# Kernel optimization log

Measured on AMD Instinct MI355X. Metric: run time of the kernel, lower is better.

The kernel has to match this reference:

```python
import jax, jax.numpy as jnp
import numpy as np

NUM_SRC = 200000
NUM_DST = 100000
NUM_EDGES = 1600000
IN_DIM = 128
HID = 256
OUT_DIM = 128


def layer_norm(h, g, b, eps=1e-5):
    mu = jnp.mean(h, axis=-1, keepdims=True)
    var = jnp.mean((h - mu) ** 2, axis=-1, keepdims=True)
    return (h - mu) * jax.lax.rsqrt(var + eps) * g + b


def setup_inputs() -> dict:
    key = jax.random.key(0)
    ks = jax.random.split(key, 8)
    s_in = 1.0 / np.sqrt(IN_DIM)
    s_hid = 1.0 / np.sqrt(HID)
    return {
        "x": jax.random.normal(ks[0], (NUM_SRC, IN_DIM), dtype=jnp.float32),
        "w_l": jax.random.normal(ks[1], (IN_DIM, HID), dtype=jnp.float32) * s_in,
        "b_l": jnp.zeros((HID,), dtype=jnp.float32),
        "w_r": jax.random.normal(ks[2], (IN_DIM, HID), dtype=jnp.float32) * s_in,
        "ln1_g": jnp.ones((HID,), dtype=jnp.float32),
        "ln1_b": jnp.zeros((HID,), dtype=jnp.float32),
        "w_out": jax.random.normal(ks[3], (HID, OUT_DIM), dtype=jnp.float32) * s_hid,
        "b_out": jnp.zeros((OUT_DIM,), dtype=jnp.float32),
        "ln2_g": jnp.ones((OUT_DIM,), dtype=jnp.float32),
        "ln2_b": jnp.zeros((OUT_DIM,), dtype=jnp.float32),
        "edge_src": jax.random.randint(ks[4], (NUM_EDGES,), 0, NUM_SRC, dtype=jnp.int64),
        "edge_dst": jax.random.randint(ks[5], (NUM_EDGES,), 0, NUM_DST, dtype=jnp.int64),
    }


def reference(x, w_l, b_l, w_r, ln1_g, ln1_b, w_out, b_out, ln2_g, ln2_b, edge_src, edge_dst):
    # SAGEConv bipartite: targets are the first NUM_DST rows of x
    x_tgt = x[:NUM_DST]
    # mean aggregation of source-node messages at destination nodes
    msgs = x[edge_src]  # [E, IN_DIM] irregular gather
    summed = jax.ops.segment_sum(msgs, edge_dst, num_segments=NUM_DST)
    cnt = jax.ops.segment_sum(jnp.ones((NUM_EDGES,), dtype=x.dtype), edge_dst, num_segments=NUM_DST)
    mean_nbr = summed / jnp.maximum(cnt, 1.0)[:, None]
    # out = lin_l(aggr) + lin_r(x_target); dropout p=0 is identity
    h = mean_nbr @ w_l + b_l + x_tgt @ w_r
    h = layer_norm(h, ln1_g, ln1_b)
    h = jax.nn.gelu(h, approximate=False)
    out = h @ w_out + b_out
    out = layer_norm(out, ln2_g, ln2_b)
    return out
```

## Files before the change

kernel.cpp:

```cpp
#include <hip/hip_runtime.h>
#include <math.h>

#define NSRC 200000
#define NDST 100000
#define NEDGE 1600000

typedef unsigned int uint32;
typedef unsigned short u16;

typedef short short8 __attribute__((ext_vector_type(8)));
typedef float f32x4 __attribute__((ext_vector_type(4)));

__device__ __forceinline__ u16 f2b(float f) {
  uint32 u = __float_as_uint(f);
  u += 0x7fffu + ((u >> 16) & 1u);
  return (u16)(u >> 16);
}
__device__ __forceinline__ float b2f_lo(uint32 u) { return __uint_as_float(u << 16); }
__device__ __forceinline__ float b2f_hi(uint32 u) { return __uint_as_float(u & 0xffff0000u); }

#define NBKT 1563
#define BKTCAP 1344
#define NB_H 256
#define EPH (NEDGE / NB_H)
#define NB_W 384
#define NB_CVT 25000

__global__ __launch_bounds__(256) void k_prep(const float* __restrict__ x, u16* __restrict__ xb,
                                              const float* __restrict__ wl,
                                              const float* __restrict__ wr,
                                              const float* __restrict__ wo,
                                              u16* __restrict__ wp1f, u16* __restrict__ wp2f,
                                              const int do_cvt, const int* __restrict__ src,
                                              const int* __restrict__ dst,
                                              int* __restrict__ bktcnt,
                                              int* __restrict__ pairs) {
  __shared__ int hist[NBKT];
  __shared__ int loff[NBKT];
  if (blockIdx.x < NB_H) {
    int base = blockIdx.x * EPH;
    for (int i = threadIdx.x; i < NBKT; i += 256) hist[i] = 0;
    __syncthreads();
    for (int i = threadIdx.x; i < EPH; i += 256) atomicAdd(&hist[dst[base + i] >> 6], 1);
    __syncthreads();
    for (int i = threadIdx.x; i < NBKT; i += 256) {
      int h = hist[i];
      loff[i] = h ? atomicAdd(&bktcnt[i * 16], h) : 0;
      hist[i] = 0;
    }
    __syncthreads();
    for (int i = threadIdx.x; i < EPH; i += 256) {
      int d = dst[base + i];
      int s = src[base + i];
      int bin = d >> 6;
      int r = atomicAdd(&hist[bin], 1);
      int pos = loff[bin] + r;
      if (pos < BKTCAP) pairs[(size_t)bin * BKTCAP + pos] = (s << 6) | (d & 63);
    }
    return;
  }
  int bid = blockIdx.x - NB_H;
  if (bid < NB_W) {
    int t = bid * 256 + threadIdx.x;
    if (t < 65536) {
      int j = t & 7, lane = (t >> 3) & 63, nt = (t >> 9) & 3, kc = (t >> 11) & 7, w = t >> 14;
      int k = kc * 32 + (lane >> 4) * 8 + j;
      int n = w * 64 + nt * 16 + (lane & 15);
      float v = (k < 128) ? wl[k * 256 + n] : wr[(k - 128) * 256 + n];
      wp1f[t] = f2b(v);
    } else {
      int t2 = t - 65536;
      int j = t2 & 7, lane = (t2 >> 3) & 63, nt = (t2 >> 9) & 1, kc = (t2 >> 10) & 7, w = t2 >> 13;
      int k = kc * 32 + (lane >> 4) * 8 + j;
      int n = w * 32 + nt * 16 + (lane & 15);
      wp2f[t2] = f2b(wo[k * 128 + n]);
    }
    return;
  }
  if (!do_cvt) return;
  int idx = (bid - NB_W) * 256 + threadIdx.x;
  size_t i = (size_t)idx * 4;
  if (i < (size_t)NSRC * 128) {
    float4 f = *(const float4*)(x + i);
    uint2 o;
    o.x = (uint32)f2b(f.x) | ((uint32)f2b(f.y) << 16);
    o.y = (uint32)f2b(f.z) | ((uint32)f2b(f.w) << 16);
    *(uint2*)(xb + i) = o;
  }
}

#define LDAH 264
#define LCSR_LD 65

__global__ __launch_bounds__(256) void k_fused(
    const u16* __restrict__ xb, const float* __restrict__ xf, const int x_is_bf16,
    const int* __restrict__ pairs, const int* __restrict__ bktcnt,
    const u16* __restrict__ wp1f, const u16* __restrict__ wp2f,
    const float* __restrict__ bl_g, const float* __restrict__ g1_g, const float* __restrict__ b1_g,
    const float* __restrict__ bo_g, const float* __restrict__ g2_g, const float* __restrict__ b2_g,
    float* __restrict__ out) {
  __shared__ __align__(16) u16 AH_lds[64 * LDAH];
  __shared__ float2 stats[4][64];
  __shared__ float2 stats2[64];
  __shared__ int lcnt[64];
  __shared__ int lcsr[64 * LCSR_LD];

  const int tid = threadIdx.x;
  const int wave = tid >> 6;
  const int lane = tid & 63;
  const int l15 = lane & 15;
  const int q = lane >> 4;
  const int row0 = blockIdx.x * 64;

  {
    const int bkt = blockIdx.x;
    int total = bktcnt[(size_t)bkt * 16];
    int mp = total < BKTCAP ? total : BKTCAP;
    if (tid < 64) lcnt[tid] = 0;
    __syncthreads();
    for (int i = tid; i < mp; i += 256) {
      int v = pairs[(size_t)bkt * BKTCAP + i];
      int d6 = v & 63;
      int p = atomicAdd(&lcnt[d6], 1);
      if (p < 64) lcsr[d6 * LCSR_LD + p] = v >> 6;
    }
    __syncthreads();
  }

  {
    const int sub = tid & 15;
    const int dgrp = tid >> 4;
#pragma unroll 1
    for (int pass = 0; pass < 4; pass++) {
      int r = pass * 16 + dgrp;
      int d = row0 + r;
      u16* rowp = AH_lds + r * LDAH;
      if (d < NDST) {
        int n = lcnt[r];
        int m = n < 64 ? n : 64;
        const int* cp = lcsr + r * LCSR_LD;
        float a[8] = {0, 0, 0, 0, 0, 0, 0, 0};
        uint4 xv;
        float4 xf0, xf1;
        if (x_is_bf16) {
          xv = *(const uint4*)(xb + (size_t)d * 128 + sub * 8);
        } else {
          const float* p = xf + (size_t)d * 128 + sub * 8;
          xf0 = *(const float4*)p;
          xf1 = *(const float4*)(p + 4);
        }
        if (x_is_bf16) {
          int i = 0;
          for (; i + 7 < m; i += 8) {
            uint4 p[8];
#pragma unroll
            for (int u = 0; u < 8; u++)
              p[u] = *(const uint4*)(xb + (size_t)cp[i + u] * 128 + sub * 8);
#pragma unroll
            for (int u = 0; u < 8; u++) {
              a[0] += b2f_lo(p[u].x); a[1] += b2f_hi(p[u].x);
              a[2] += b2f_lo(p[u].y); a[3] += b2f_hi(p[u].y);
              a[4] += b2f_lo(p[u].z); a[5] += b2f_hi(p[u].z);
              a[6] += b2f_lo(p[u].w); a[7] += b2f_hi(p[u].w);
            }
          }
          for (; i + 3 < m; i += 4) {
            uint4 p[4];
#pragma unroll
            for (int u = 0; u < 4; u++)
              p[u] = *(const uint4*)(xb + (size_t)cp[i + u] * 128 + sub * 8);
#pragma unroll
            for (int u = 0; u < 4; u++) {
              a[0] += b2f_lo(p[u].x); a[1] += b2f_hi(p[u].x);
              a[2] += b2f_lo(p[u].y); a[3] += b2f_hi(p[u].y);
              a[4] += b2f_lo(p[u].z); a[5] += b2f_hi(p[u].z);
              a[6] += b2f_lo(p[u].w); a[7] += b2f_hi(p[u].w);
            }
          }
          for (; i < m; i++) {
            uint4 p = *(const uint4*)(xb + (size_t)cp[i] * 128 + sub * 8);
            a[0] += b2f_lo(p.x); a[1] += b2f_hi(p.x);
            a[2] += b2f_lo(p.y); a[3] += b2f_hi(p.y);
            a[4] += b2f_lo(p.z); a[5] += b2f_hi(p.z);
            a[6] += b2f_lo(p.w); a[7] += b2f_hi(p.w);
          }
        } else {
          for (int i = 0; i < m; i++) {
            int s = cp[i];
            const float* p = xf + (size_t)s * 128 + sub * 8;
            float4 f0 = *(const float4*)p;
            float4 f1 = *(const float4*)(p + 4);
            a[0] += f0.x; a[1] += f0.y; a[2] += f0.z; a[3] += f0.w;
            a[4] += f1.x; a[5] += f1.y; a[6] += f1.z; a[7] += f1.w;
          }
        }
        float sc = 1.f / (float)(n > 0 ? n : 1);
        uint4 o;
        o.x = (uint32)f2b(a[0] * sc) | ((uint32)f2b(a[1] * sc) << 16);
        o.y = (uint32)f2b(a[2] * sc) | ((uint32)f2b(a[3] * sc) << 16);
        o.z = (uint32)f2b(a[4] * sc) | ((uint32)f2b(a[5] * sc) << 16);
        o.w = (uint32)f2b(a[6] * sc) | ((uint32)f2b(a[7] * sc) << 16);
        *(uint4*)(rowp + sub * 8) = o;
        if (!x_is_bf16) {
          xv.x = (uint32)f2b(xf0.x) | ((uint32)f2b(xf0.y) << 16);
          xv.y = (uint32)f2b(xf0.z) | ((uint32)f2b(xf0.w) << 16);
          xv.z = (uint32)f2b(xf1.x) | ((uint32)f2b(xf1.y) << 16);
          xv.w = (uint32)f2b(xf1.z) | ((uint32)f2b(xf1.w) << 16);
        }
        *(uint4*)(rowp + 128 + sub * 8) = xv;
      } else {
        uint4 z = {0u, 0u, 0u, 0u};
        *(uint4*)(rowp + sub * 8) = z;
        *(uint4*)(rowp + 128 + sub * 8) = z;
      }
    }
  }
  __syncthreads();

  f32x4 acc[4][4];
#pragma unroll
  for (int i = 0; i < 4; i++)
#pragma unroll
    for (int j = 0; j < 4; j++) acc[i][j] = (f32x4){0.f, 0.f, 0.f, 0.f};

#pragma unroll 2
  for (int kc = 0; kc < 8; kc++) {
    short8 bfr[4];
    const uint4* bsrc = (const uint4*)(wp1f + (((size_t)wave * 8 + kc) * 4) * 512);
#pragma unroll
    for (int nt = 0; nt < 4; nt++) bfr[nt] = ((const short8*)(bsrc + nt * 64))[lane];
    short8 af[4];
#pragma unroll
    for (int mt = 0; mt < 4; mt++)
      af[mt] = *(const short8*)(AH_lds + (16 * mt + l15) * LDAH + kc * 32 + q * 8);
#pragma unroll
    for (int mt = 0; mt < 4; mt++)
#pragma unroll
      for (int nt = 0; nt < 4; nt++)
        acc[mt][nt] = __builtin_amdgcn_mfma_f32_16x16x32_bf16(af[mt], bfr[nt], acc[mt][nt], 0, 0, 0);
  }

  float bl[4], g1[4], b1[4];
#pragma unroll
  for (int nt = 0; nt < 4; nt++) {
    int c = 64 * wave + 16 * nt + l15;
    bl[nt] = bl_g[c]; g1[nt] = g1_g[c]; b1[nt] = b1_g[c];
  }
#pragma unroll
  for (int mt = 0; mt < 4; mt++)
#pragma unroll
    for (int nt = 0; nt < 4; nt++)
#pragma unroll
      for (int r = 0; r < 4; r++) acc[mt][nt][r] += bl[nt];

#pragma unroll
  for (int mt = 0; mt < 4; mt++)
#pragma unroll
    for (int r = 0; r < 4; r++) {
      float s = 0.f, s2 = 0.f;
#pragma unroll
      for (int nt = 0; nt < 4; nt++) { float v = acc[mt][nt][r]; s += v; s2 += v * v; }
#pragma unroll
      for (int m = 1; m < 16; m <<= 1) { s += __shfl_xor(s, m, 64); s2 += __shfl_xor(s2, m, 64); }
      if (l15 == 0) stats[wave][16 * mt + 4 * q + r] = make_float2(s, s2);
    }
  __syncthreads();
  if (tid < 64) {
    float S = 0.f, Q = 0.f;
#pragma unroll
    for (int w = 0; w < 4; w++) { float2 t = stats[w][tid]; S += t.x; Q += t.y; }
    float mu = S * (1.f / 256.f);
    float var = Q * (1.f / 256.f) - mu * mu;
    stats2[tid] = make_float2(mu, rsqrtf(var + 1e-5f));
  }
  __syncthreads();
#pragma unroll
  for (int mt = 0; mt < 4; mt++)
#pragma unroll
    for (int r = 0; r < 4; r++) {
      int row = 16 * mt + 4 * q + r;
      float2 st = stats2[row];
#pragma unroll
      for (int nt = 0; nt < 4; nt++) {
        float v = acc[mt][nt][r];
        float hn = (v - st.x) * st.y * g1[nt] + b1[nt];
        float t2 = hn * hn;
        float u = fmaf(0.044715f * t2, hn, hn);
        float ge = hn / (1.f + __expf(-1.5957691216f * u));
        AH_lds[row * LDAH + 64 * wave + 16 * nt + l15] = f2b(ge);
      }
    }
  __syncthreads();

  f32x4 acc2[4][2];
#pragma unroll
  for (int i = 0; i < 4; i++)
#pragma unroll
    for (int j = 0; j < 2; j++) acc2[i][j] = (f32x4){0.f, 0.f, 0.f, 0.f};

#pragma unroll 2
  for (int kc = 0; kc < 8; kc++) {
    short8 bfr[2];
    const uint4* bsrc = (const uint4*)(wp2f + (((size_t)wave * 8 + kc) * 2) * 512);
#pragma unroll
    for (int nt = 0; nt < 2; nt++) bfr[nt] = ((const short8*)(bsrc + nt * 64))[lane];
    short8 af[4];
#pragma unroll
    for (int mt = 0; mt < 4; mt++)
      af[mt] = *(const short8*)(AH_lds + (16 * mt + l15) * LDAH + kc * 32 + q * 8);
#pragma unroll
    for (int mt = 0; mt < 4; mt++)
#pragma unroll
      for (int nt = 0; nt < 2; nt++)
        acc2[mt][nt] = __builtin_amdgcn_mfma_f32_16x16x32_bf16(af[mt], bfr[nt], acc2[mt][nt], 0, 0, 0);
  }

  float bo[2], g2[2], b2c[2];
#pragma unroll
  for (int nt = 0; nt < 2; nt++) {
    int c = 32 * wave + 16 * nt + l15;
    bo[nt] = bo_g[c]; g2[nt] = g2_g[c]; b2c[nt] = b2_g[c];
  }
#pragma unroll
  for (int mt = 0; mt < 4; mt++)
#pragma unroll
    for (int nt = 0; nt < 2; nt++)
#pragma unroll
      for (int r = 0; r < 4; r++) acc2[mt][nt][r] += bo[nt];

#pragma unroll
  for (int mt = 0; mt < 4; mt++)
#pragma unroll
    for (int r = 0; r < 4; r++) {
      float s = 0.f, s2 = 0.f;
#pragma unroll
      for (int nt = 0; nt < 2; nt++) { float v = acc2[mt][nt][r]; s += v; s2 += v * v; }
#pragma unroll
      for (int m = 1; m < 16; m <<= 1) { s += __shfl_xor(s, m, 64); s2 += __shfl_xor(s2, m, 64); }
      if (l15 == 0) stats[wave][16 * mt + 4 * q + r] = make_float2(s, s2);
    }
  __syncthreads();
  if (tid < 64) {
    float S = 0.f, Q = 0.f;
#pragma unroll
    for (int w = 0; w < 4; w++) { float2 t = stats[w][tid]; S += t.x; Q += t.y; }
    float mu = S * (1.f / 128.f);
    float var = Q * (1.f / 128.f) - mu * mu;
    stats2[tid] = make_float2(mu, rsqrtf(var + 1e-5f));
  }
  __syncthreads();
#pragma unroll
  for (int mt = 0; mt < 4; mt++)
#pragma unroll
    for (int r = 0; r < 4; r++) {
      int row = 16 * mt + 4 * q + r;
      int R = row0 + row;
      if (R < NDST) {
        float2 st = stats2[row];
#pragma unroll
        for (int nt = 0; nt < 2; nt++) {
          float v = acc2[mt][nt][r];
          out[(size_t)R * 128 + 32 * wave + 16 * nt + l15] = (v - st.x) * st.y * g2[nt] + b2c[nt];
        }
      }
    }
}

extern "C" void kernel_launch(void* const* d_in, const int* in_sizes, int n_in,
                              void* d_out, int out_size, void* d_ws, size_t ws_size,
                              hipStream_t stream) {
  const float* x   = (const float*)d_in[0];
  const float* w_l = (const float*)d_in[1];
  const float* b_l = (const float*)d_in[2];
  const float* w_r = (const float*)d_in[3];
  const float* g1  = (const float*)d_in[4];
  const float* b1  = (const float*)d_in[5];
  const float* w_o = (const float*)d_in[6];
  const float* b_o = (const float*)d_in[7];
  const float* g2  = (const float*)d_in[8];
  const float* b2  = (const float*)d_in[9];
  const int* esrc  = (const int*)d_in[10];
  const int* edst  = (const int*)d_in[11];
  float* out = (float*)d_out;

  char* ws = (char*)d_ws;
  size_t off = 0;
  auto alloc = [&](size_t bytes) -> void* {
    off = (off + 255) & ~(size_t)255;
    void* p = ws + off;
    off += bytes;
    return p;
  };
  int* bktcnt = (int*)alloc((size_t)NBKT * 16 * 4);
  u16* wp1f   = (u16*)alloc((size_t)65536 * 2);
  u16* wp2f   = (u16*)alloc((size_t)32768 * 2);
  int* pairs  = (int*)alloc((size_t)NBKT * BKTCAP * 4);

  size_t rem = (ws_size > off + 512) ? (ws_size - off - 512) : 0;
  size_t xb_bytes = (size_t)NSRC * 128 * 2;
  int x_is_bf16 = (rem >= xb_bytes) ? 1 : 0;
  u16* xb = x_is_bf16 ? (u16*)alloc(xb_bytes) : nullptr;

  hipMemsetAsync(bktcnt, 0, (size_t)NBKT * 16 * 4, stream);
  k_prep<<<NB_H + NB_W + NB_CVT, 256, 0, stream>>>(x, xb, w_l, w_r, w_o, wp1f, wp2f,
                                                   x_is_bf16, esrc, edst, bktcnt, pairs);
  k_fused<<<NBKT, 256, 0, stream>>>(xb, x, x_is_bf16, pairs, bktcnt, wp1f, wp2f,
                                    b_l, g1, b1, b_o, g2, b2, out);
}
```

Before: 368.5 us.

## Use 512-thread blocks with 2x4 wave grid in fused SAGE kernel

Doubles the fused kernel's block size to 8 waves. The 64-row tile is split into two 32-row halves across wave rows, so each wave holds half the accumulators and the gather loop runs two passes instead of four. Per-row LayerNorm stats are reorganized into an 8x32 layout. The intent is more gather parallelism per bucket and lower register pressure, which should raise occupancy. The cost is that each wave now reloads the same B-fragment weights for only half the M-tiles, and more threads take part in each barrier.

After: 355.6 us. -3.5%, faster.

```diff
diff --git a/kernel.cpp b/kernel.cpp
--- a/kernel.cpp
+++ b/kernel.cpp
@@ -92,7 +92,7 @@
 #define LDAH 264
 #define LCSR_LD 65
 
-__global__ __launch_bounds__(256) void k_fused(
+__global__ __launch_bounds__(512, 6) void k_fused(
     const u16* __restrict__ xb, const float* __restrict__ xf, const int x_is_bf16,
     const int* __restrict__ pairs, const int* __restrict__ bktcnt,
     const u16* __restrict__ wp1f, const u16* __restrict__ wp2f,
@@ -100,7 +100,7 @@
     const float* __restrict__ bo_g, const float* __restrict__ g2_g, const float* __restrict__ b2_g,
     float* __restrict__ out) {
   __shared__ __align__(16) u16 AH_lds[64 * LDAH];
-  __shared__ float2 stats[4][64];
+  __shared__ float2 stats[8][32];
   __shared__ float2 stats2[64];
   __shared__ int lcnt[64];
   __shared__ int lcsr[64 * LCSR_LD];
@@ -110,6 +110,8 @@
   const int lane = tid & 63;
   const int l15 = lane & 15;
   const int q = lane >> 4;
+  const int wr = wave >> 2;
+  const int wc = wave & 3;
   const int row0 = blockIdx.x * 64;
 
   {
@@ -118,7 +120,7 @@
     int mp = total < BKTCAP ? total : BKTCAP;
     if (tid < 64) lcnt[tid] = 0;
     __syncthreads();
-    for (int i = tid; i < mp; i += 256) {
+    for (int i = tid; i < mp; i += 512) {
       int v = pairs[(size_t)bkt * BKTCAP + i];
       int d6 = v & 63;
       int p = atomicAdd(&lcnt[d6], 1);
@@ -131,8 +133,8 @@
     const int sub = tid & 15;
     const int dgrp = tid >> 4;
 #pragma unroll 1
-    for (int pass = 0; pass < 4; pass++) {
-      int r = pass * 16 + dgrp;
+    for (int pass = 0; pass < 2; pass++) {
+      int r = pass * 32 + dgrp;
       int d = row0 + r;
       u16* rowp = AH_lds + r * LDAH;
       if (d < NDST) {
@@ -217,24 +219,24 @@
   }
   __syncthreads();
 
-  f32x4 acc[4][4];
-#pragma unroll
-  for (int i = 0; i < 4; i++)
+  f32x4 acc[2][4];
+#pragma unroll
+  for (int i = 0; i < 2; i++)
 #pragma unroll
     for (int j = 0; j < 4; j++) acc[i][j] = (f32x4){0.f, 0.f, 0.f, 0.f};
 
-#pragma unroll 2
+#pragma unroll 1
   for (int kc = 0; kc < 8; kc++) {
     short8 bfr[4];
-    const uint4* bsrc = (const uint4*)(wp1f + (((size_t)wave * 8 + kc) * 4) * 512);
+    const uint4* bsrc = (const uint4*)(wp1f + (((size_t)wc * 8 + kc) * 4) * 512);
 #pragma unroll
     for (int nt = 0; nt < 4; nt++) bfr[nt] = ((const short8*)(bsrc + nt * 64))[lane];
-    short8 af[4];
-#pragma unroll
-    for (int mt = 0; mt < 4; mt++)
-      af[mt] = *(const short8*)(AH_lds + (16 * mt + l15) * LDAH + kc * 32 + q * 8);
-#pragma unroll
-    for (int mt = 0; mt < 4; mt++)
+    short8 af[2];
+#pragma unroll
+    for (int mt = 0; mt < 2; mt++)
+      af[mt] = *(const short8*)(AH_lds + (32 * wr + 16 * mt + l15) * LDAH + kc * 32 + q * 8);
+#pragma unroll
+    for (int mt = 0; mt < 2; mt++)
 #pragma unroll
       for (int nt = 0; nt < 4; nt++)
         acc[mt][nt] = __builtin_amdgcn_mfma_f32_16x16x32_bf16(af[mt], bfr[nt], acc[mt][nt], 0, 0, 0);
@@ -243,18 +245,18 @@
   float bl[4], g1[4], b1[4];
 #pragma unroll
   for (int nt = 0; nt < 4; nt++) {
-    int c = 64 * wave + 16 * nt + l15;
+    int c = 64 * wc + 16 * nt + l15;
     bl[nt] = bl_g[c]; g1[nt] = g1_g[c]; b1[nt] = b1_g[c];
   }
 #pragma unroll
-  for (int mt = 0; mt < 4; mt++)
+  for (int mt = 0; mt < 2; mt++)
 #pragma unroll
     for (int nt = 0; nt < 4; nt++)
 #pragma unroll
       for (int r = 0; r < 4; r++) acc[mt][nt][r] += bl[nt];
 
 #pragma unroll
-  for (int mt = 0; mt < 4; mt++)
+  for (int mt = 0; mt < 2; mt++)
 #pragma unroll
     for (int r = 0; r < 4; r++) {
       float s = 0.f, s2 = 0.f;
@@ -266,19 +268,20 @@
     }
   __syncthreads();
   if (tid < 64) {
+    int wr_ = tid >> 5, rl = tid & 31;
     float S = 0.f, Q = 0.f;
 #pragma unroll
-    for (int w = 0; w < 4; w++) { float2 t = stats[w][tid]; S += t.x; Q += t.y; }
+    for (int w = 0; w < 4; w++) { float2 t = stats[wr_ * 4 + w][rl]; S += t.x; Q += t.y; }
     float mu = S * (1.f / 256.f);
     float var = Q * (1.f / 256.f) - mu * mu;
     stats2[tid] = make_float2(mu, rsqrtf(var + 1e-5f));
   }
   __syncthreads();
 #pragma unroll
-  for (int mt = 0; mt < 4; mt++)
+  for (int mt = 0; mt < 2; mt++)
 #pragma unroll
     for (int r = 0; r < 4; r++) {
-      int row = 16 * mt + 4 * q + r;
+      int row = 32 * wr + 16 * mt + 4 * q + r;
       float2 st = stats2[row];
 #pragma unroll
       for (int nt = 0; nt < 4; nt++) {
@@ -287,29 +290,29 @@
         float t2 = hn * hn;
         float u = fmaf(0.044715f * t2, hn, hn);
         float ge = hn / (1.f + __expf(-1.5957691216f * u));
-        AH_lds[row * LDAH + 64 * wave + 16 * nt + l15] = f2b(ge);
+        AH_lds[row * LDAH + 64 * wc + 16 * nt + l15] = f2b(ge);
       }
     }
   __syncthreads();
 
-  f32x4 acc2[4][2];
-#pragma unroll
-  for (int i = 0; i < 4; i++)
+  f32x4 acc2[2][2];
+#pragma unroll
+  for (int i = 0; i < 2; i++)
 #pragma unroll
     for (int j = 0; j < 2; j++) acc2[i][j] = (f32x4){0.f, 0.f, 0.f, 0.f};
 
-#pragma unroll 2
+#pragma unroll 1
   for (int kc = 0; kc < 8; kc++) {
     short8 bfr[2];
-    const uint4* bsrc = (const uint4*)(wp2f + (((size_t)wave * 8 + kc) * 2) * 512);
+    const uint4* bsrc = (const uint4*)(wp2f + (((size_t)wc * 8 + kc) * 2) * 512);
 #pragma unroll
     for (int nt = 0; nt < 2; nt++) bfr[nt] = ((const short8*)(bsrc + nt * 64))[lane];
-    short8 af[4];
-#pragma unroll
-    for (int mt = 0; mt < 4; mt++)
-      af[mt] = *(const short8*)(AH_lds + (16 * mt + l15) * LDAH + kc * 32 + q * 8);
-#pragma unroll
-    for (int mt = 0; mt < 4; mt++)
+    short8 af[2];
+#pragma unroll
+    for (int mt = 0; mt < 2; mt++)
+      af[mt] = *(const short8*)(AH_lds + (32 * wr + 16 * mt + l15) * LDAH + kc * 32 + q * 8);
+#pragma unroll
+    for (int mt = 0; mt < 2; mt++)
 #pragma unroll
       for (int nt = 0; nt < 2; nt++)
         acc2[mt][nt] = __builtin_amdgcn_mfma_f32_16x16x32_bf16(af[mt], bfr[nt], acc2[mt][nt], 0, 0, 0);
@@ -318,18 +321,18 @@
   float bo[2], g2[2], b2c[2];
 #pragma unroll
   for (int nt = 0; nt < 2; nt++) {
-    int c = 32 * wave + 16 * nt + l15;
+    int c = 32 * wc + 16 * nt + l15;
     bo[nt] = bo_g[c]; g2[nt] = g2_g[c]; b2c[nt] = b2_g[c];
   }
 #pragma unroll
-  for (int mt = 0; mt < 4; mt++)
+  for (int mt = 0; mt < 2; mt++)
 #pragma unroll
     for (int nt = 0; nt < 2; nt++)
 #pragma unroll
       for (int r = 0; r < 4; r++) acc2[mt][nt][r] += bo[nt];
 
 #pragma unroll
-  for (int mt = 0; mt < 4; mt++)
+  for (int mt = 0; mt < 2; mt++)
 #pragma unroll
     for (int r = 0; r < 4; r++) {
       float s = 0.f, s2 = 0.f;
@@ -341,26 +344,27 @@
     }
   __syncthreads();
   if (tid < 64) {
+    int wr_ = tid >> 5, rl = tid & 31;
     float S = 0.f, Q = 0.f;
 #pragma unroll
-    for (int w = 0; w < 4; w++) { float2 t = stats[w][tid]; S += t.x; Q += t.y; }
+    for (int w = 0; w < 4; w++) { float2 t = stats[wr_ * 4 + w][rl]; S += t.x; Q += t.y; }
     float mu = S * (1.f / 128.f);
     float var = Q * (1.f / 128.f) - mu * mu;
     stats2[tid] = make_float2(mu, rsqrtf(var + 1e-5f));
   }
   __syncthreads();
 #pragma unroll
-  for (int mt = 0; mt < 4; mt++)
+  for (int mt = 0; mt < 2; mt++)
 #pragma unroll
     for (int r = 0; r < 4; r++) {
-      int row = 16 * mt + 4 * q + r;
+      int row = 32 * wr + 16 * mt + 4 * q + r;
       int R = row0 + row;
       if (R < NDST) {
         float2 st = stats2[row];
 #pragma unroll
         for (int nt = 0; nt < 2; nt++) {
           float v = acc2[mt][nt][r];
-          out[(size_t)R * 128 + 32 * wave + 16 * nt + l15] = (v - st.x) * st.y * g2[nt] + b2c[nt];
+          out[(size_t)R * 128 + 32 * wc + 16 * nt + l15] = (v - st.x) * st.y * g2[nt] + b2c[nt];
         }
       }
     }
@@ -404,6 +408,6 @@
   hipMemsetAsync(bktcnt, 0, (size_t)NBKT * 16 * 4, stream);
   k_prep<<<NB_H + NB_W + NB_CVT, 256, 0, stream>>>(x, xb, w_l, w_r, w_o, wp1f, wp2f,
                                                    x_is_bf16, esrc, edst, bktcnt, pairs);
-  k_fused<<<NBKT, 256, 0, stream>>>(xb, x, x_is_bf16, pairs, bktcnt, wp1f, wp2f,
+  k_fused<<<NBKT, 512, 0, stream>>>(xb, x, x_is_bf16, pairs, bktcnt, wp1f, wp2f,
                                     b_l, g1, b1, b_o, g2, b2, out);
 }
```
